# Kernel optimization log

Measured on AMD Instinct MI355X. Metric: run time of the kernel, lower is better.

The kernel has to match this reference:

```python
import jax, jax.numpy as jnp
import numpy as np

N_NODES = 50000
N_EDGES = 1_600_000
D = 128


def setup_inputs() -> dict:
    key = jax.random.key(0)
    k1, k2, k3 = jax.random.split(key, 3)
    x = jax.random.normal(k1, (N_NODES, D), dtype=jnp.float32)
    edge_index = jax.random.randint(k2, (2, N_EDGES), 0, N_NODES, dtype=jnp.int64)
    W = jax.random.normal(k3, (D, D), dtype=jnp.float32) / np.sqrt(D)
    b = jnp.zeros((D,), dtype=jnp.float32)
    return {"x": x, "edge_index": edge_index, "W": W, "b": b}


def _sgconv(x, src, dst, W, b, n):
    # gcn_norm with self-loops: D^{-1/2} (A + I) D^{-1/2}
    loop = jnp.arange(n, dtype=src.dtype)
    src = jnp.concatenate([src, loop])
    dst = jnp.concatenate([dst, loop])
    ones = jnp.ones(src.shape[0], dtype=x.dtype)
    deg = jax.ops.segment_sum(ones, dst, num_segments=n)  # in-degree incl. self-loop
    dinv = jnp.where(deg > 0, jax.lax.rsqrt(deg), jnp.zeros_like(deg))
    norm = dinv[src] * dinv[dst]                      # [E+N]
    msg = x[src] * norm[:, None]                      # gather + scale, [E+N, D]
    agg = jax.ops.segment_sum(msg, dst, num_segments=n)  # scatter-add, [N, D]
    return agg @ W.T + b                              # SGConv linear (K=1)


def reference(x, edge_index, W, b):
    n = x.shape[0]
    h = _sgconv(x, edge_index[0], edge_index[1], W, b, n)
    return x + jax.nn.relu(h)
```

## Files before the change

kernel.cpp:

```cpp
#include <hip/hip_runtime.h>
#include <hip/hip_fp16.h>

#define D 128
#define BSHIFT 6
#define BSIZE 64
#define NBMAX 1024
#define BCAP 3072
#define PA_BLOCKS 256
#define OVF_CAP 65536
#define GB_THREADS 1024

using half8 = __attribute__((ext_vector_type(8))) _Float16;
using float4v = __attribute__((ext_vector_type(4))) float;
using floatx2 = __attribute__((ext_vector_type(2))) float;

__global__ __launch_bounds__(256) void histA_kernel(const int* __restrict__ dst,
                                                    int* __restrict__ ph, int E, int NB) {
    __shared__ int hist[NBMAX];
    int t = threadIdx.x;
    for (int b = t; b < NB; b += 256) hist[b] = 0;
    __syncthreads();
    int chunk = (((E + (int)gridDim.x - 1) / (int)gridDim.x) + 3) & ~3;
    int start = blockIdx.x * chunk;
    int end = min(start + chunk, E);
    for (int i = start + 4 * t; i < end; i += 4 * 256) {
        if (i + 3 < end) {
            int4 v = *(const int4*)&dst[i];
            atomicAdd(&hist[v.x >> BSHIFT], 1);
            atomicAdd(&hist[v.y >> BSHIFT], 1);
            atomicAdd(&hist[v.z >> BSHIFT], 1);
            atomicAdd(&hist[v.w >> BSHIFT], 1);
        } else {
            for (int j = i; j < end; ++j) atomicAdd(&hist[dst[j] >> BSHIFT], 1);
        }
    }
    __syncthreads();
    int* row = ph + (size_t)blockIdx.x * NB;
    for (int b = t; b < NB; b += 256) row[b] = hist[b];
}

__global__ __launch_bounds__(PA_BLOCKS) void scanA_kernel(int* __restrict__ ph,
                                                          int* __restrict__ bucket_cnt,
                                                          int NB) {
    __shared__ int sh[PA_BLOCKS];
    int b = blockIdx.x;
    int t = threadIdx.x;
    int v = ph[(size_t)t * NB + b];
    sh[t] = v;
    __syncthreads();
    for (int off = 1; off < PA_BLOCKS; off <<= 1) {
        int add = (t >= off) ? sh[t - off] : 0;
        __syncthreads();
        sh[t] += add;
        __syncthreads();
    }
    ph[(size_t)t * NB + b] = sh[t] - v;
    if (t == PA_BLOCKS - 1) bucket_cnt[b] = sh[t];
}

__global__ __launch_bounds__(256) void placeA_kernel(const int* __restrict__ src,
                                                     const int* __restrict__ dst,
                                                     const int* __restrict__ ph,
                                                     int* __restrict__ pairs,
                                                     int* __restrict__ ovfA_cnt,
                                                     int2* __restrict__ ovfA,
                                                     int E, int NB) {
    __shared__ int sbase[NBMAX];
    __shared__ int cur[NBMAX];
    int t = threadIdx.x;
    const int* row = ph + (size_t)blockIdx.x * NB;
    for (int b = t; b < NB; b += 256) { sbase[b] = row[b]; cur[b] = 0; }
    __syncthreads();
    int chunk = (((E + (int)gridDim.x - 1) / (int)gridDim.x) + 3) & ~3;
    int start = blockIdx.x * chunk;
    int end = min(start + chunk, E);

    auto place = [&](int dd, int ss) {
        int b = dd >> BSHIFT;
        int p = sbase[b] + atomicAdd(&cur[b], 1);
        if (p < BCAP) {
            pairs[(size_t)b * BCAP + p] = (ss << BSHIFT) | (dd & (BSIZE - 1));
        } else {
            int q = atomicAdd(ovfA_cnt, 1);
            if (q < OVF_CAP) ovfA[q] = make_int2(dd, ss);
        }
    };

    for (int i = start + 4 * t; i < end; i += 4 * 256) {
        if (i + 3 < end) {
            int4 dv = *(const int4*)&dst[i];
            int4 sv = *(const int4*)&src[i];
            place(dv.x, sv.x);
            place(dv.y, sv.y);
            place(dv.z, sv.z);
            place(dv.w, sv.w);
        } else {
            for (int j = i; j < end; ++j) place(dst[j], src[j]);
        }
    }
}

__global__ __launch_bounds__(256) void xw_kernel(const float* __restrict__ x,
                                                 const float* __restrict__ W,
                                                 const int* __restrict__ pairs,
                                                 const int* __restrict__ bucket_cnt,
                                                 const int* __restrict__ ovfA_cnt,
                                                 const int2* __restrict__ ovfA,
                                                 unsigned char* __restrict__ xw, int N) {
    __shared__ _Float16 Bf[128 * 128];
    __shared__ int degX[BSIZE];
    const int t = threadIdx.x;
    const int b = blockIdx.x;
    if (t < BSIZE) degX[t] = 0;
    __syncthreads();

    {
        int cnt = min(bucket_cnt[b], BCAP);
        const int* pp = pairs + (size_t)b * BCAP;
        for (int i = t; i < cnt; i += 256) atomicAdd(&degX[pp[i] & (BSIZE - 1)], 1);
        int na = *ovfA_cnt;
        if (na > 0) {
            if (na > OVF_CAP) na = OVF_CAP;
            for (int k = t; k < na; k += 256) {
                int dd = ovfA[k].x;
                if ((dd >> BSHIFT) == b) atomicAdd(&degX[dd & (BSIZE - 1)], 1);
            }
        }
    }

    {
        int n = t >> 1;
        int jt = n >> 4, nlo = n & 15;
        int kbase = (t & 1) * 64;
#pragma unroll
        for (int o = 0; o < 8; ++o) {
            int k0 = kbase + o * 8;
            float4 f0 = *(const float4*)&W[n * 128 + k0];
            float4 f1 = *(const float4*)&W[n * 128 + k0 + 4];
            int kt = k0 >> 5, quad = (k0 >> 3) & 3;
            half8 h;
            h[0] = (_Float16)f0.x; h[1] = (_Float16)f0.y;
            h[2] = (_Float16)f0.z; h[3] = (_Float16)f0.w;
            h[4] = (_Float16)f1.x; h[5] = (_Float16)f1.y;
            h[6] = (_Float16)f1.z; h[7] = (_Float16)f1.w;
            *(half8*)&Bf[(size_t)(((kt * 8 + jt) * 4 + quad) * 16 + nlo) * 8] = h;
        }
    }
    __syncthreads();

    const int wave = t >> 6, lane = t & 63;
    const int quad = lane >> 4, nlo = lane & 15;
    const int r0 = b * 64 + wave * 16;
    const int rA = r0 + nlo;
    const int rAc = (rA < N) ? rA : (N - 1);
    const float dv = rsqrtf((float)degX[rAc - b * 64] + 1.0f);

    float4v acc[8];
#pragma unroll
    for (int j = 0; j < 8; ++j) acc[j] = (float4v){0.f, 0.f, 0.f, 0.f};

#pragma unroll
    for (int kt = 0; kt < 4; ++kt) {
        const float* xp = x + (size_t)rAc * D + kt * 32 + quad * 8;
        float4 a0 = *(const float4*)xp;
        float4 a1 = *(const float4*)(xp + 4);
        half8 va;
        va[0] = (_Float16)(a0.x * dv); va[1] = (_Float16)(a0.y * dv);
        va[2] = (_Float16)(a0.z * dv); va[3] = (_Float16)(a0.w * dv);
        va[4] = (_Float16)(a1.x * dv); va[5] = (_Float16)(a1.y * dv);
        va[6] = (_Float16)(a1.z * dv); va[7] = (_Float16)(a1.w * dv);
#pragma unroll
        for (int jt = 0; jt < 8; ++jt) {
            half8 vb = *(half8*)&Bf[(size_t)((kt * 8 + jt) * 64 + lane) * 8];
            acc[jt] = __builtin_amdgcn_mfma_f32_16x16x32_f16(va, vb, acc[jt], 0, 0, 0);
        }
    }

#pragma unroll
    for (int reg = 0; reg < 4; ++reg) {
        int row = r0 + quad * 4 + reg;
        if (row < N) {
            int u0 = __builtin_amdgcn_cvt_pk_fp8_f32(acc[0][reg], acc[1][reg], 0, false);
            u0 = __builtin_amdgcn_cvt_pk_fp8_f32(acc[2][reg], acc[3][reg], u0, true);
            int u1 = __builtin_amdgcn_cvt_pk_fp8_f32(acc[4][reg], acc[5][reg], 0, false);
            u1 = __builtin_amdgcn_cvt_pk_fp8_f32(acc[6][reg], acc[7][reg], u1, true);
            *(uint2*)(xw + (size_t)row * 128 + nlo * 8) = make_uint2((unsigned)u0, (unsigned)u1);
        }
    }
}

__global__ __launch_bounds__(GB_THREADS) void gatherB_kernel(
    const float* __restrict__ x, const unsigned char* __restrict__ xw,
    const int* __restrict__ pairs, const int* __restrict__ bucket_cnt,
    const float* __restrict__ bias, const int* __restrict__ ovfA_cnt,
    const int2* __restrict__ ovfA, float* __restrict__ out, int N) {
    __shared__ int lds_src[BCAP];
    __shared__ int degL[BSIZE], offs[BSIZE], cur[BSIZE], spillc[BSIZE];
    const int b = blockIdx.x;
    const int t = threadIdx.x;
    if (t < BSIZE) { degL[t] = 0; cur[t] = 0; spillc[t] = 0; }
    __syncthreads();
    const int cnt = min(bucket_cnt[b], BCAP);
    int na = *ovfA_cnt;
    if (na > OVF_CAP) na = OVF_CAP;

    int my_w[3], my_n = 0;
    for (int i = t; i < cnt; i += GB_THREADS) {
        int w = pairs[(size_t)b * BCAP + i];
        my_w[my_n++] = w;
        atomicAdd(&degL[w & (BSIZE - 1)], 1);
    }
    if (na > 0) {
        for (int k = t; k < na; k += GB_THREADS) {
            int dd = ovfA[k].x;
            if ((dd >> BSHIFT) == b) atomicAdd(&spillc[dd & (BSIZE - 1)], 1);
        }
    }
    __syncthreads();

    if (t < BSIZE) {
        int v = degL[t];
        int s = v;
#pragma unroll
        for (int o = 1; o < 64; o <<= 1) {
            int u = __shfl_up(s, o, 64);
            if (t >= o) s += u;
        }
        offs[t] = s - v;
    }
    __syncthreads();

    for (int k = 0; k < my_n; ++k) {
        int w = my_w[k];
        int dl = w & (BSIZE - 1);
        int p = atomicAdd(&cur[dl], 1);
        lds_src[offs[dl] + p] = w >> BSHIFT;
    }
    __syncthreads();

    const int wave = t >> 6, lane = t & 63;
    const int half = lane >> 5, c31 = lane & 31;
    const unsigned int* xw32 = (const unsigned int*)xw;

    int col[4];
    float bcol[4];
#pragma unroll
    for (int k = 0; k < 4; ++k) {
        int s = 4 * c31 + k;
        col[k] = ((s & 7) << 4) + (s >> 3);
        bcol[k] = bias[col[k]];
    }

    for (int q = 0; q < 4; ++q) {
        int dl = wave * 4 + q;
        int node = b * BSIZE + dl;
        if (node >= N) break;
        int start = offs[dl];
        int end = start + degL[dl];
        float dvd = rsqrtf((float)(degL[dl] + spillc[dl]) + 1.0f);
        size_t noff = (size_t)node * D;

        float a0 = 0.f, a1 = 0.f, a2 = 0.f, a3 = 0.f;

        int e = start;
        for (; e + 7 < end; e += 8) {
            int r0 = lds_src[e + 0 + half], r1 = lds_src[e + 2 + half];
            int r2 = lds_src[e + 4 + half], r3 = lds_src[e + 6 + half];
            unsigned int w0 = xw32[(size_t)r0 * 32 + c31];
            unsigned int w1 = xw32[(size_t)r1 * 32 + c31];
            unsigned int w2 = xw32[(size_t)r2 * 32 + c31];
            unsigned int w3 = xw32[(size_t)r3 * 32 + c31];
            floatx2 l0 = __builtin_amdgcn_cvt_pk_f32_fp8((int)w0, false);
            floatx2 h0 = __builtin_amdgcn_cvt_pk_f32_fp8((int)w0, true);
            floatx2 l1 = __builtin_amdgcn_cvt_pk_f32_fp8((int)w1, false);
            floatx2 h1 = __builtin_amdgcn_cvt_pk_f32_fp8((int)w1, true);
            floatx2 l2 = __builtin_amdgcn_cvt_pk_f32_fp8((int)w2, false);
            floatx2 h2 = __builtin_amdgcn_cvt_pk_f32_fp8((int)w2, true);
            floatx2 l3 = __builtin_amdgcn_cvt_pk_f32_fp8((int)w3, false);
            floatx2 h3 = __builtin_amdgcn_cvt_pk_f32_fp8((int)w3, true);
            a0 += (l0.x + l1.x) + (l2.x + l3.x);
            a1 += (l0.y + l1.y) + (l2.y + l3.y);
            a2 += (h0.x + h1.x) + (h2.x + h3.x);
            a3 += (h0.y + h1.y) + (h2.y + h3.y);
        }
        for (; e + 1 < end; e += 2) {
            int r = lds_src[e + half];
            unsigned int w = xw32[(size_t)r * 32 + c31];
            floatx2 lo = __builtin_amdgcn_cvt_pk_f32_fp8((int)w, false);
            floatx2 hi = __builtin_amdgcn_cvt_pk_f32_fp8((int)w, true);
            a0 += lo.x; a1 += lo.y; a2 += hi.x; a3 += hi.y;
        }
        if (e < end && half == 0) {
            int r = lds_src[e];
            unsigned int w = xw32[(size_t)r * 32 + c31];
            floatx2 lo = __builtin_amdgcn_cvt_pk_f32_fp8((int)w, false);
            floatx2 hi = __builtin_amdgcn_cvt_pk_f32_fp8((int)w, true);
            a0 += lo.x; a1 += lo.y; a2 += hi.x; a3 += hi.y;
        }

        a0 += __shfl_xor(a0, 32);
        a1 += __shfl_xor(a1, 32);
        a2 += __shfl_xor(a2, 32);
        a3 += __shfl_xor(a3, 32);

        if (half == 0) {
            unsigned int ws = xw32[(size_t)node * 32 + c31];
            floatx2 lo = __builtin_amdgcn_cvt_pk_f32_fp8((int)ws, false);
            floatx2 hi = __builtin_amdgcn_cvt_pk_f32_fp8((int)ws, true);
            a0 += lo.x; a1 += lo.y; a2 += hi.x; a3 += hi.y;
            if (na > 0) {
                for (int k = 0; k < na; ++k) {
                    int2 pr = ovfA[k];
                    if (pr.x == node) {
                        unsigned int w = xw32[(size_t)pr.y * 32 + c31];
                        floatx2 l2_ = __builtin_amdgcn_cvt_pk_f32_fp8((int)w, false);
                        floatx2 h2_ = __builtin_amdgcn_cvt_pk_f32_fp8((int)w, true);
                        a0 += l2_.x; a1 += l2_.y; a2 += h2_.x; a3 += h2_.y;
                    }
                }
            }
            float h0 = a0 * dvd + bcol[0];
            float h1 = a1 * dvd + bcol[1];
            float h2 = a2 * dvd + bcol[2];
            float h3 = a3 * dvd + bcol[3];
            out[noff + col[0]] = x[noff + col[0]] + (h0 > 0.f ? h0 : 0.f);
            out[noff + col[1]] = x[noff + col[1]] + (h1 > 0.f ? h1 : 0.f);
            out[noff + col[2]] = x[noff + col[2]] + (h2 > 0.f ? h2 : 0.f);
            out[noff + col[3]] = x[noff + col[3]] + (h3 > 0.f ? h3 : 0.f);
        }
    }
}

extern "C" void kernel_launch(void* const* d_in, const int* in_sizes, int n_in,
                              void* d_out, int out_size, void* d_ws, size_t ws_size,
                              hipStream_t stream) {
    const float* x = (const float*)d_in[0];
    const int* ei = (const int*)d_in[1];
    const float* W = (const float*)d_in[2];
    const float* bias = (const float*)d_in[3];
    float* out = (float*)d_out;

    const int N = in_sizes[0] / D;
    const int E = in_sizes[1] / 2;
    const int* src = ei;
    const int* dst = ei + E;
    const int NB = (N + BSIZE - 1) / BSIZE;

    char* p = (char*)d_ws;
    int* pairs = (int*)p;            p += (size_t)NB * BCAP * sizeof(int);
    unsigned char* xw = (unsigned char*)p; p += (size_t)N * 128;
    int* bucket_cnt = (int*)p;       p += (size_t)NBMAX * sizeof(int);
    int* ovfA_cnt = (int*)p;         p += 16;
    int2* ovfA = (int2*)p;           p += (size_t)OVF_CAP * sizeof(int2);
    int* ph = (int*)p;               p += (size_t)PA_BLOCKS * NB * sizeof(int);

    hipMemsetAsync(ovfA_cnt, 0, 16, stream);

    histA_kernel<<<PA_BLOCKS, 256, 0, stream>>>(dst, ph, E, NB);
    scanA_kernel<<<NB, PA_BLOCKS, 0, stream>>>(ph, bucket_cnt, NB);
    placeA_kernel<<<PA_BLOCKS, 256, 0, stream>>>(src, dst, ph, pairs,
                                                 ovfA_cnt, ovfA, E, NB);
    xw_kernel<<<NB, 256, 0, stream>>>(x, W, pairs, bucket_cnt, ovfA_cnt, ovfA, xw, N);
    gatherB_kernel<<<NB, GB_THREADS, 0, stream>>>(x, xw, pairs, bucket_cnt,
                                                  bias, ovfA_cnt, ovfA, out, N);
}
```

Baseline: 161.7 us.

## Fuse histogram, scan and placement into one kernel using global atomic bucket reservation

Replaces the three-kernel bucketing pipeline (per-block histogram, cross-block scan, placement) with a single prep kernel. Each block builds its local histogram, then reserves a contiguous range per bucket with one global atomicAdd on bucket_cnt before placing edges. This removes two launches and the per-block histogram round trip through global memory, at the cost of a nondeterministic edge order within buckets. The epilogue of the gather kernel is also changed so both wave halves each finish two of the four columns instead of one half doing all four.

```diff
diff --git a/kernel.cpp b/kernel.cpp
--- a/kernel.cpp
+++ b/kernel.cpp
@@ -6,7 +6,7 @@
 #define BSIZE 64
 #define NBMAX 1024
 #define BCAP 3072
-#define PA_BLOCKS 256
+#define PREP_BLOCKS 256
 #define OVF_CAP 65536
 #define GB_THREADS 1024
 
@@ -14,66 +14,41 @@
 using float4v = __attribute__((ext_vector_type(4))) float;
 using floatx2 = __attribute__((ext_vector_type(2))) float;
 
-__global__ __launch_bounds__(256) void histA_kernel(const int* __restrict__ dst,
-                                                    int* __restrict__ ph, int E, int NB) {
-    __shared__ int hist[NBMAX];
-    int t = threadIdx.x;
-    for (int b = t; b < NB; b += 256) hist[b] = 0;
-    __syncthreads();
+__global__ __launch_bounds__(256) void prep_kernel(const int* __restrict__ src,
+                                                   const int* __restrict__ dst,
+                                                   int* __restrict__ bucket_cnt,
+                                                   int* __restrict__ pairs,
+                                                   int* __restrict__ ovfA_cnt,
+                                                   int2* __restrict__ ovfA,
+                                                   int E, int NB) {
+    __shared__ int sbase[NBMAX];
+    __shared__ int cur[NBMAX];
+    const int t = threadIdx.x;
+    for (int b = t; b < NB; b += 256) { sbase[b] = 0; cur[b] = 0; }
+    __syncthreads();
+
     int chunk = (((E + (int)gridDim.x - 1) / (int)gridDim.x) + 3) & ~3;
     int start = blockIdx.x * chunk;
     int end = min(start + chunk, E);
+
     for (int i = start + 4 * t; i < end; i += 4 * 256) {
         if (i + 3 < end) {
             int4 v = *(const int4*)&dst[i];
-            atomicAdd(&hist[v.x >> BSHIFT], 1);
-            atomicAdd(&hist[v.y >> BSHIFT], 1);
-            atomicAdd(&hist[v.z >> BSHIFT], 1);
-            atomicAdd(&hist[v.w >> BSHIFT], 1);
+            atomicAdd(&sbase[v.x >> BSHIFT], 1);
+            atomicAdd(&sbase[v.y >> BSHIFT], 1);
+            atomicAdd(&sbase[v.z >> BSHIFT], 1);
+            atomicAdd(&sbase[v.w >> BSHIFT], 1);
         } else {
-            for (int j = i; j < end; ++j) atomicAdd(&hist[dst[j] >> BSHIFT], 1);
-        }
-    }
-    __syncthreads();
-    int* row = ph + (size_t)blockIdx.x * NB;
-    for (int b = t; b < NB; b += 256) row[b] = hist[b];
-}
-
-__global__ __launch_bounds__(PA_BLOCKS) void scanA_kernel(int* __restrict__ ph,
-                                                          int* __restrict__ bucket_cnt,
-                                                          int NB) {
-    __shared__ int sh[PA_BLOCKS];
-    int b = blockIdx.x;
-    int t = threadIdx.x;
-    int v = ph[(size_t)t * NB + b];
-    sh[t] = v;
-    __syncthreads();
-    for (int off = 1; off < PA_BLOCKS; off <<= 1) {
-        int add = (t >= off) ? sh[t - off] : 0;
-        __syncthreads();
-        sh[t] += add;
-        __syncthreads();
-    }
-    ph[(size_t)t * NB + b] = sh[t] - v;
-    if (t == PA_BLOCKS - 1) bucket_cnt[b] = sh[t];
-}
-
-__global__ __launch_bounds__(256) void placeA_kernel(const int* __restrict__ src,
-                                                     const int* __restrict__ dst,
-                                                     const int* __restrict__ ph,
-                                                     int* __restrict__ pairs,
-                                                     int* __restrict__ ovfA_cnt,
-                                                     int2* __restrict__ ovfA,
-                                                     int E, int NB) {
-    __shared__ int sbase[NBMAX];
-    __shared__ int cur[NBMAX];
-    int t = threadIdx.x;
-    const int* row = ph + (size_t)blockIdx.x * NB;
-    for (int b = t; b < NB; b += 256) { sbase[b] = row[b]; cur[b] = 0; }
-    __syncthreads();
-    int chunk = (((E + (int)gridDim.x - 1) / (int)gridDim.x) + 3) & ~3;
-    int start = blockIdx.x * chunk;
-    int end = min(start + chunk, E);
+            for (int j = i; j < end; ++j) atomicAdd(&sbase[dst[j] >> BSHIFT], 1);
+        }
+    }
+    __syncthreads();
+
+    for (int b = t; b < NB; b += 256) {
+        int h = sbase[b];
+        sbase[b] = h ? atomicAdd(&bucket_cnt[b], h) : 0;
+    }
+    __syncthreads();
 
     auto place = [&](int dd, int ss) {
         int b = dd >> BSHIFT;
@@ -303,31 +278,28 @@
         a2 += __shfl_xor(a2, 32);
         a3 += __shfl_xor(a3, 32);
 
-        if (half == 0) {
-            unsigned int ws = xw32[(size_t)node * 32 + c31];
-            floatx2 lo = __builtin_amdgcn_cvt_pk_f32_fp8((int)ws, false);
-            floatx2 hi = __builtin_amdgcn_cvt_pk_f32_fp8((int)ws, true);
-            a0 += lo.x; a1 += lo.y; a2 += hi.x; a3 += hi.y;
+        float s0 = half ? a2 : a0;
+        float s1 = half ? a3 : a1;
+        {
+            unsigned int ws = xw32[(size_t)node * 32 + c31] >> (half * 16);
+            floatx2 sv = __builtin_amdgcn_cvt_pk_f32_fp8((int)ws, false);
+            s0 += sv.x; s1 += sv.y;
             if (na > 0) {
                 for (int k = 0; k < na; ++k) {
                     int2 pr = ovfA[k];
                     if (pr.x == node) {
-                        unsigned int w = xw32[(size_t)pr.y * 32 + c31];
-                        floatx2 l2_ = __builtin_amdgcn_cvt_pk_f32_fp8((int)w, false);
-                        floatx2 h2_ = __builtin_amdgcn_cvt_pk_f32_fp8((int)w, true);
-                        a0 += l2_.x; a1 += l2_.y; a2 += h2_.x; a3 += h2_.y;
+                        unsigned int w = xw32[(size_t)pr.y * 32 + c31] >> (half * 16);
+                        floatx2 v2 = __builtin_amdgcn_cvt_pk_f32_fp8((int)w, false);
+                        s0 += v2.x; s1 += v2.y;
                     }
                 }
             }
-            float h0 = a0 * dvd + bcol[0];
-            float h1 = a1 * dvd + bcol[1];
-            float h2 = a2 * dvd + bcol[2];
-            float h3 = a3 * dvd + bcol[3];
-            out[noff + col[0]] = x[noff + col[0]] + (h0 > 0.f ? h0 : 0.f);
-            out[noff + col[1]] = x[noff + col[1]] + (h1 > 0.f ? h1 : 0.f);
-            out[noff + col[2]] = x[noff + col[2]] + (h2 > 0.f ? h2 : 0.f);
-            out[noff + col[3]] = x[noff + col[3]] + (h3 > 0.f ? h3 : 0.f);
-        }
+        }
+        int c0 = col[2 * half], c1 = col[2 * half + 1];
+        float h0 = s0 * dvd + bcol[2 * half];
+        float h1 = s1 * dvd + bcol[2 * half + 1];
+        out[noff + c0] = x[noff + c0] + (h0 > 0.f ? h0 : 0.f);
+        out[noff + c1] = x[noff + c1] + (h1 > 0.f ? h1 : 0.f);
     }
 }
 
@@ -352,13 +324,10 @@
     int* bucket_cnt = (int*)p;       p += (size_t)NBMAX * sizeof(int);
     int* ovfA_cnt = (int*)p;         p += 16;
     int2* ovfA = (int2*)p;           p += (size_t)OVF_CAP * sizeof(int2);
-    int* ph = (int*)p;               p += (size_t)PA_BLOCKS * NB * sizeof(int);
-
-    hipMemsetAsync(ovfA_cnt, 0, 16, stream);
-
-    histA_kernel<<<PA_BLOCKS, 256, 0, stream>>>(dst, ph, E, NB);
-    scanA_kernel<<<NB, PA_BLOCKS, 0, stream>>>(ph, bucket_cnt, NB);
-    placeA_kernel<<<PA_BLOCKS, 256, 0, stream>>>(src, dst, ph, pairs,
+
+    hipMemsetAsync(bucket_cnt, 0, (size_t)NBMAX * sizeof(int) + 16, stream);
+
+    prep_kernel<<<PREP_BLOCKS, 256, 0, stream>>>(src, dst, bucket_cnt, pairs,
                                                  ovfA_cnt, ovfA, E, NB);
     xw_kernel<<<NB, 256, 0, stream>>>(x, W, pairs, bucket_cnt, ovfA_cnt, ovfA, xw, N);
     gatherB_kernel<<<NB, GB_THREADS, 0, stream>>>(x, xw, pairs, bucket_cnt,
```

Result: faster. 156.9 us (-3.0%).
